# Performance work log

Measured on AMD Instinct MI355X. Metric: run time of the kernel, lower is better.

## Reference

```python
import jax, jax.numpy as jnp
import numpy as np

N, E, D_IN, D_HID, D_OUT = 50000, 800000, 128, 128, 64

def setup_inputs() -> dict:
    key = jax.random.key(0)
    ks = jax.random.split(key, 20)
    inp = {
        'x': jax.random.normal(ks[0], (N, D_IN), dtype=jnp.float32),
        'edge_index': jax.random.randint(ks[1], (2, E), 0, N, dtype=jnp.int64),
        'edge_attr': jax.random.normal(ks[2], (E, 16), dtype=jnp.float32),
        'edge_weight': jax.random.uniform(ks[3], (E,), dtype=jnp.float32),
    }
    dims = [(D_IN, D_HID), (D_HID, D_HID), (D_HID, D_OUT)]
    for i, (di, do) in enumerate(dims):
        s = 1.0 / np.sqrt(di)
        inp[f'Wl{i}'] = jax.random.uniform(ks[4 + 5 * i], (di, do), minval=-s, maxval=s, dtype=jnp.float32)
        inp[f'bl{i}'] = jnp.zeros((do,), dtype=jnp.float32)
        inp[f'Wr{i}'] = jax.random.uniform(ks[5 + 5 * i], (di, do), minval=-s, maxval=s, dtype=jnp.float32)
        inp[f'Ws{i}'] = jax.random.uniform(ks[6 + 5 * i], (di, do), minval=-s, maxval=s, dtype=jnp.float32)
        inp[f'bs{i}'] = jnp.zeros((do,), dtype=jnp.float32)
    return inp


def _sage(x, src, dst, Wl, bl, Wr):
    # mean aggregation of source features at target nodes (PyG SAGEConv)
    msg = x[src]                                               # [E, d] gather
    ssum = jax.ops.segment_sum(msg, dst, num_segments=N)        # [N, d]
    cnt = jax.ops.segment_sum(jnp.ones((src.shape[0],), x.dtype), dst, num_segments=N)
    agg = ssum / jnp.maximum(cnt, 1.0)[:, None]
    return agg @ Wl + bl + x @ Wr                               # lin_l(agg) + lin_r(x)


def reference(x, edge_index, edge_attr, edge_weight,
              Wl0, bl0, Wr0, Ws0, bs0,
              Wl1, bl1, Wr1, Ws1, bs1,
              Wl2, bl2, Wr2, Ws2, bs2):
    src, dst = edge_index[0], edge_index[1]
    h = jax.nn.relu(_sage(x, src, dst, Wl0, bl0, Wr0) + x @ Ws0 + bs0)
    h = jax.nn.relu(_sage(h, src, dst, Wl1, bl1, Wr1) + h @ Ws1 + bs1)
    out = _sage(h, src, dst, Wl2, bl2, Wr2) + h @ Ws2 + bs2
    return out
```

## Files before the change

kernel.cpp:

```cpp
#include <hip/hip_runtime.h>
#include <hip/hip_bf16.h>


#define LB __launch_bounds__

typedef __attribute__((ext_vector_type(8))) short short8;
typedef __attribute__((ext_vector_type(4))) float f32x4;

__device__ __forceinline__ unsigned short bf16_rne(float f) {
  unsigned u = __builtin_bit_cast(unsigned, f);
  unsigned r = u + 0x7fffu + ((u >> 16) & 1u);
  return (unsigned short)(r >> 16);
}
__device__ __forceinline__ float bf16_to_f(unsigned short us) {
  return __builtin_bit_cast(float, (unsigned)us << 16);
}
__device__ __forceinline__ float bits_to_f(unsigned u) {
  return __builtin_bit_cast(float, u);
}

__device__ __forceinline__ void async16(const void* g, void* l) {
  __builtin_amdgcn_global_load_lds((const __attribute__((address_space(1))) unsigned*)g,
                                   (__attribute__((address_space(3))) unsigned*)l, 16, 0, 0);
}

#define BCAP 8192
#define P1_CHUNK 4096

__device__ __forceinline__ void p1_body(int bid, const int* __restrict__ src,
                                        const int* __restrict__ dst, int* __restrict__ bcnt,
                                        int2* __restrict__ pairs, int E) {
  __shared__ int cnt[256];
  __shared__ int base[256];
  const int tid = threadIdx.x;
  cnt[tid] = 0;
  __syncthreads();
  const int e0 = bid * P1_CHUNK;
  int myb[16], myr[16], mys[16], myd[16];
#pragma unroll
  for (int i = 0; i < 16; ++i) {
    int e = e0 + i * 256 + tid;
    myb[i] = -1;
    if (e < E) {
      int s = src[e], d = dst[e];
      int b = d >> 8;
      myb[i] = b;
      mys[i] = s;
      myd[i] = d;
      myr[i] = atomicAdd(&cnt[b], 1);
    }
  }
  __syncthreads();
  base[tid] = (cnt[tid] > 0) ? atomicAdd(&bcnt[tid], cnt[tid]) : 0;
  __syncthreads();
#pragma unroll
  for (int i = 0; i < 16; ++i) {
    int b = myb[i];
    if (b >= 0) {
      int p = base[b] + myr[i];
      if (p < BCAP) pairs[(size_t)b * BCAP + p] = make_int2(mys[i], myd[i]);
    }
  }
}

__device__ __forceinline__ void p234_body(int b, const int2* __restrict__ pairs,
                                          const int* __restrict__ bcnt, int* __restrict__ gcounter,
                                          int* __restrict__ row_start, int* __restrict__ deg_arr,
                                          float* __restrict__ scale, int* __restrict__ srcs, int N) {
  __shared__ int h[256];
  __shared__ int sc[256];
  __shared__ int cur[256];
  __shared__ int shared_bb;
  const int tid = threadIdx.x;
  h[tid] = 0;
  __syncthreads();
  int m = bcnt[b];
  if (m > BCAP) m = BCAP;
  for (int i = tid; i < m; i += 256) {
    atomicAdd(&h[pairs[(size_t)b * BCAP + i].y & 255], 1);
  }
  __syncthreads();
  const int deg = h[tid];
  sc[tid] = deg;
  __syncthreads();
  for (int off = 1; off < 256; off <<= 1) {
    int add = (tid >= off) ? sc[tid - off] : 0;
    __syncthreads();
    sc[tid] += add;
    __syncthreads();
  }
  if (tid == 0) shared_bb = atomicAdd(gcounter, sc[255]);
  __syncthreads();
  const int abs_off = shared_bb + sc[tid] - deg;
  const int node = b * 256 + tid;
  if (node < N) {
    row_start[node] = abs_off;
    deg_arr[node] = deg;
    scale[node] = 1.0f / (float)(deg > 1 ? deg : 1);
  }
  cur[tid] = abs_off;
  __syncthreads();
  for (int i = tid; i < m; i += 256) {
    int2 pr = pairs[(size_t)b * BCAP + i];
    int p = atomicAdd(&cur[pr.y & 255], 1);
    srcs[p] = pr.x;
  }
}

__device__ __forceinline__ void wpack_body(int wb, const float* __restrict__ Wl0,
                                           const float* __restrict__ Wr0,
                                           const float* __restrict__ Ws0,
                                           const float* __restrict__ bl0,
                                           const float* __restrict__ bs0,
                                           const float* __restrict__ Wl1,
                                           const float* __restrict__ Wr1,
                                           const float* __restrict__ Ws1,
                                           const float* __restrict__ bl1,
                                           const float* __restrict__ bs1,
                                           const float* __restrict__ Wl2,
                                           const float* __restrict__ Wr2,
                                           const float* __restrict__ Ws2,
                                           const float* __restrict__ bl2,
                                           const float* __restrict__ bs2, ushort* __restrict__ Bh0,
                                           ushort* __restrict__ Bo0, float* __restrict__ bb0,
                                           ushort* __restrict__ Bh1, ushort* __restrict__ Bo1,
                                           float* __restrict__ bb1, ushort* __restrict__ Bh2,
                                           ushort* __restrict__ Bo2, float* __restrict__ bb2) {
  const int layer = wb >> 7;
  const int xb = wb & 127;
  const float *Wl, *Wr, *Ws, *bl, *bs;
  ushort *Bh, *Bo;
  float* bb;
  int M;
  if (layer == 0) {
    Wl = Wl0; Wr = Wr0; Ws = Ws0; bl = bl0; bs = bs0; Bh = Bh0; Bo = Bo0; bb = bb0; M = 256;
  } else if (layer == 1) {
    Wl = Wl1; Wr = Wr1; Ws = Ws1; bl = bl1; bs = bs1; Bh = Bh1; Bo = Bo1; bb = bb1; M = 256;
  } else {
    Wl = Wl2; Wr = Wr2; Ws = Ws2; bl = bl2; bs = bs2; Bh = Bh2; Bo = Bo2; bb = bb2; M = 128;
  }
  const int DO = M / 2;
  int idx = xb * 256 + (int)threadIdx.x;
  if (idx < 128 * M) {
    int k = idx / M, c = idx - k * M;
    float v = (c < DO) ? Wl[k * DO + c] : (Wr[k * DO + (c - DO)] + Ws[k * DO + (c - DO)]);
    unsigned short h = bf16_rne(v);
    unsigned short l = bf16_rne(v - bf16_to_f(h));
    int d = ((k >> 3) * M + c) * 8 + (k & 7);
    Bh[d] = h;
    Bo[d] = l;
  }
  if (idx < DO) bb[idx] = bl[idx] + bs[idx];
}

__device__ __forceinline__ void split8v(f32x4 f0, f32x4 f1, short8& h, short8& l) {
  float f[8] = {f0[0], f0[1], f0[2], f0[3], f1[0], f1[1], f1[2], f1[3]};
#pragma unroll
  for (int j = 0; j < 8; ++j) {
    unsigned u = __builtin_bit_cast(unsigned, f[j]);
    h[j] = (short)(u >> 16);
    l[j] = (short)bf16_rne(f[j] - bits_to_f(u & 0xffff0000u));
  }
}

template <int M>
__device__ __forceinline__ void gemm_compute(int bx, const char* smem,
                                             const ushort* __restrict__ Bhi,
                                             const ushort* __restrict__ Blo,
                                             ushort* __restrict__ Yb, float* __restrict__ Z,
                                             int n) {
  constexpr int DO = M / 2;
  constexpr int NWC = (M >= 256) ? 4 : 2;
  constexpr int NWR = 4 / NWC;
  constexpr int BROWS = 32 * NWR;
  const int tid = threadIdx.x;
  const int w = tid >> 6, l = tid & 63;
  const int q = l >> 4, m16 = l & 15;
  const int rowBase = bx * BROWS + (w / NWC) * 32;
  const int colBase = (w % NWC) * 64;

  f32x4 acc[2][4] = {};
  const int rl0 = (w / NWC) * 32 + m16;

#pragma unroll
  for (int s = 0; s < 4; ++s) {
    short8 ah[2], al[2], bh[4], bo[4];
    const int kb = s * 4 + q;
#pragma unroll
    for (int i = 0; i < 2; ++i) {
      int rl = rl0 + i * 16;
      int g0 = (2 * kb) ^ m16;
      int g1 = (2 * kb + 1) ^ m16;
      f32x4 fa = *(const f32x4*)(smem + (size_t)rl * 512 + g0 * 16);
      f32x4 fb = *(const f32x4*)(smem + (size_t)rl * 512 + g1 * 16);
      split8v(fa, fb, ah[i], al[i]);
    }
#pragma unroll
    for (int j = 0; j < 4; ++j) {
      size_t off = ((size_t)kb * M + colBase + j * 16 + m16) * 8;
      bh[j] = *(const short8*)(Bhi + off);
      bo[j] = *(const short8*)(Blo + off);
    }
#pragma unroll
    for (int i = 0; i < 2; ++i)
#pragma unroll
      for (int j = 0; j < 4; ++j) {
        acc[i][j] = __builtin_amdgcn_mfma_f32_16x16x32_bf16(ah[i], bh[j], acc[i][j], 0, 0, 0);
        acc[i][j] = __builtin_amdgcn_mfma_f32_16x16x32_bf16(ah[i], bo[j], acc[i][j], 0, 0, 0);
        acc[i][j] = __builtin_amdgcn_mfma_f32_16x16x32_bf16(al[i], bh[j], acc[i][j], 0, 0, 0);
      }
  }

#pragma unroll
  for (int i = 0; i < 2; ++i) {
    int rb = rowBase + i * 16 + q * 4;
#pragma unroll
    for (int j = 0; j < 4; ++j) {
      int c = colBase + j * 16 + m16;
#pragma unroll
      for (int r = 0; r < 4; ++r) {
        int row = rb + r;
        if (row < n) {
          float v = acc[i][j][r];
          if (c < DO)
            Yb[(size_t)row * DO + c] = bf16_rne(v);
          else
            Z[(size_t)row * DO + (c - DO)] = v;
        }
      }
    }
  }
}

__device__ __forceinline__ void gemm0_body(int bx, const float* __restrict__ x,
                                           const ushort* __restrict__ Bh,
                                           const ushort* __restrict__ Bo, ushort* __restrict__ Yb,
                                           float* __restrict__ Z, int n, char* smem) {
  const int tid = threadIdx.x;
  const int wbase = tid & ~63;
#pragma unroll
  for (int r = 0; r < 4; ++r) {
    int ell = r * 256 + tid;
    int row = ell >> 5, gl = ell & 31;
    int grow = bx * 32 + row;
    if (grow >= n) grow = n - 1;
    int gs = gl ^ (row & 15);
    async16(x + (size_t)grow * 128 + gs * 4, smem + (size_t)(r * 256 + wbase) * 16);
  }
  __syncthreads();
  gemm_compute<256>(bx, smem, Bh, Bo, Yb, Z, n);
}

__device__ __forceinline__ void acc8(float* a, uint4 u) {
  a[0] += bits_to_f(u.x << 16);
  a[1] += bits_to_f(u.x & 0xffff0000u);
  a[2] += bits_to_f(u.y << 16);
  a[3] += bits_to_f(u.y & 0xffff0000u);
  a[4] += bits_to_f(u.z << 16);
  a[5] += bits_to_f(u.z & 0xffff0000u);
  a[6] += bits_to_f(u.w << 16);
  a[7] += bits_to_f(u.w & 0xffff0000u);
}

template <int M>
__global__ LB(256, 4) void fused_agg_gemm(const ushort* __restrict__ Y,
                                          const float* __restrict__ Zprev,
                                          const int* __restrict__ row_start,
                                          const int* __restrict__ deg_arr,
                                          const int* __restrict__ srcs,
                                          const float* __restrict__ scale,
                                          const float* __restrict__ bsum,
                                          const ushort* __restrict__ Bhi,
                                          const ushort* __restrict__ Blo, ushort* __restrict__ Yb,
                                          float* __restrict__ Zf, int n) {
  constexpr int BROWS = (M >= 256) ? 32 : 64;
  __shared__ __align__(16) char smem[BROWS * 512];
  const int tid = threadIdx.x;
  const int w = tid >> 6;
  const int lane = tid & 63;
  const int qt = lane >> 4;
  const int li = lane & 15;
  const int blockRow0 = blockIdx.x * BROWS;
  const uint4* Y4 = (const uint4*)Y;

#pragma unroll 1
  for (int t = 0; t < BROWS / 16; ++t) {
    const int r = t * 16 + w * 4 + qt;
    const int node = blockRow0 + r;
    const bool live = node < n;
    const int cn = live ? node : n - 1;
    const int e0q = row_start[cn];
    const int cntq = live ? deg_arr[cn] : 0;
    const float sc = scale[cn];
    float4 z0 = ((const float4*)Zprev)[(size_t)cn * 32 + 2 * li];
    float4 z1 = ((const float4*)Zprev)[(size_t)cn * 32 + 2 * li + 1];
    float4 b0 = ((const float4*)bsum)[2 * li];
    float4 b1 = ((const float4*)bsum)[2 * li + 1];
    float a[8] = {0.f, 0.f, 0.f, 0.f, 0.f, 0.f, 0.f, 0.f};

    int cm = cntq;
    cm = max(cm, __shfl_xor(cm, 16));
    cm = max(cm, __shfl_xor(cm, 32));

    for (int base = 0; base < cm; base += 16) {
      int idx = (base + li < cntq) ? srcs[e0q + base + li] : 0;
      int lim = cm - base;
      if (lim > 16) lim = 16;
      for (int jj = 0; jj < lim; jj += 8) {
        int s[8];
#pragma unroll
        for (int k = 0; k < 8; ++k) s[k] = __shfl(idx, (qt << 4) + jj + k);
        uint4 u[8];
#pragma unroll
        for (int k = 0; k < 8; ++k) {
          uint4 v = make_uint4(0u, 0u, 0u, 0u);
          if (base + jj + k < cntq) v = Y4[(size_t)s[k] * 16 + li];
          u[k] = v;
        }
#pragma unroll
        for (int k = 0; k < 8; ++k) acc8(a, u[k]);
      }
    }
    float4 o0, o1;
    o0.x = fmaxf(z0.x + sc * a[0] + b0.x, 0.f);
    o0.y = fmaxf(z0.y + sc * a[1] + b0.y, 0.f);
    o0.z = fmaxf(z0.z + sc * a[2] + b0.z, 0.f);
    o0.w = fmaxf(z0.w + sc * a[3] + b0.w, 0.f);
    o1.x = fmaxf(z1.x + sc * a[4] + b1.x, 0.f);
    o1.y = fmaxf(z1.y + sc * a[5] + b1.y, 0.f);
    o1.z = fmaxf(z1.z + sc * a[6] + b1.z, 0.f);
    o1.w = fmaxf(z1.w + sc * a[7] + b1.w, 0.f);
    *(float4*)(smem + (size_t)r * 512 + (size_t)(((2 * li) ^ (r & 15)) * 16)) = o0;
    *(float4*)(smem + (size_t)r * 512 + (size_t)(((2 * li + 1) ^ (r & 15)) * 16)) = o1;
  }
  __syncthreads();
  gemm_compute<M>(blockIdx.x, smem, Bhi, Blo, Yb, Zf, n);
}

__global__ LB(256) void fused_wpack_p1(const int* __restrict__ src, const int* __restrict__ dst,
                                       int* __restrict__ bcnt, int2* __restrict__ pairs, int E,
                                       int NP1, const float* Wl0, const float* Wr0, const float* Ws0,
                                       const float* bl0, const float* bs0, const float* Wl1,
                                       const float* Wr1, const float* Ws1, const float* bl1,
                                       const float* bs1, const float* Wl2, const float* Wr2,
                                       const float* Ws2, const float* bl2, const float* bs2,
                                       ushort* Bh0, ushort* Bo0, float* bb0, ushort* Bh1,
                                       ushort* Bo1, float* bb1, ushort* Bh2, ushort* Bo2,
                                       float* bb2) {
  if ((int)blockIdx.x < NP1) {
    p1_body(blockIdx.x, src, dst, bcnt, pairs, E);
  } else {
    wpack_body(blockIdx.x - NP1, Wl0, Wr0, Ws0, bl0, bs0, Wl1, Wr1, Ws1, bl1, bs1, Wl2, Wr2, Ws2,
               bl2, bs2, Bh0, Bo0, bb0, Bh1, Bo1, bb1, Bh2, Bo2, bb2);
  }
}

__global__ LB(256, 5) void fused_p234_gemm0(const int2* __restrict__ pairs,
                                            const int* __restrict__ bcnt, int* __restrict__ gcounter,
                                            int* __restrict__ row_start, int* __restrict__ deg_arr,
                                            float* __restrict__ scale, int* __restrict__ srcs, int N,
                                            const float* __restrict__ x,
                                            const ushort* __restrict__ Bh0,
                                            const ushort* __restrict__ Bo0, ushort* __restrict__ Yb,
                                            float* __restrict__ Zf, int NB) {
  __shared__ __align__(16) char smem[32 * 512];
  if ((int)blockIdx.x < NB) {
    p234_body(blockIdx.x, pairs, bcnt, gcounter, row_start, deg_arr, scale, srcs, N);
  } else {
    gemm0_body(blockIdx.x - NB, x, Bh0, Bo0, Yb, Zf, N, smem);
  }
}

__global__ LB(256, 4) void agg64_kernel(const ushort* __restrict__ Y, const float* __restrict__ Z,
                                        const int* __restrict__ row_start,
                                        const int* __restrict__ deg_arr, const int* __restrict__ srcs,
                                        const float* __restrict__ scale,
                                        const float* __restrict__ bsum, float* __restrict__ out,
                                        int n) {
  const int tid = threadIdx.x;
  const int lane = tid & 63;
  const int qt = lane >> 4;
  const int li = lane & 15;
  const int node = blockIdx.x * 16 + (tid >> 6) * 4 + qt;
  const bool live = node < n;
  const int cn = live ? node : n - 1;
  const int e0q = row_start[cn];
  const int cntq = live ? deg_arr[cn] : 0;
  const uint2* Yu = (const uint2*)Y;
  float a0 = 0.f, a1 = 0.f, a2 = 0.f, a3 = 0.f;
  const float sc = scale[cn];
  float4 z = ((const float4*)Z)[(size_t)cn * 16 + li];
  float4 b = ((const float4*)bsum)[li];

  int cm = cntq;
  cm = max(cm, __shfl_xor(cm, 16));
  cm = max(cm, __shfl_xor(cm, 32));

  for (int base = 0; base < cm; base += 16) {
    int idx = (base + li < cntq) ? srcs[e0q + base + li] : 0;
    int lim = cm - base;
    if (lim > 16) lim = 16;
    for (int jj = 0; jj < lim; jj += 8) {
      int s[8];
#pragma unroll
      for (int k = 0; k < 8; ++k) s[k] = __shfl(idx, (qt << 4) + jj + k);
      uint2 u[8];
#pragma unroll
      for (int k = 0; k < 8; ++k) {
        uint2 v = make_uint2(0u, 0u);
        if (base + jj + k < cntq) v = Yu[(size_t)s[k] * 16 + li];
        u[k] = v;
      }
#pragma unroll
      for (int k = 0; k < 8; ++k) {
        a0 += bits_to_f(u[k].x << 16);
        a1 += bits_to_f(u[k].x & 0xffff0000u);
        a2 += bits_to_f(u[k].y << 16);
        a3 += bits_to_f(u[k].y & 0xffff0000u);
      }
    }
  }
  if (live) {
    float4 o;
    o.x = z.x + sc * a0 + b.x;
    o.y = z.y + sc * a1 + b.y;
    o.z = z.z + sc * a2 + b.z;
    o.w = z.w + sc * a3 + b.w;
    ((float4*)out)[(size_t)node * 16 + li] = o;
  }
}

extern "C" void kernel_launch(void* const* d_in, const int* in_sizes, int n_in,
                              void* d_out, int out_size, void* d_ws, size_t ws_size,
                              hipStream_t stream) {
  const float* x = (const float*)d_in[0];
  const int* ei = (const int*)d_in[1];
  const int N = in_sizes[0] / 128;
  const int E = in_sizes[3];
  const int* src = ei;
  const int* dst = ei + E;
  const float* Wl[3] = {(const float*)d_in[4], (const float*)d_in[9], (const float*)d_in[14]};
  const float* bl[3] = {(const float*)d_in[5], (const float*)d_in[10], (const float*)d_in[15]};
  const float* Wr[3] = {(const float*)d_in[6], (const float*)d_in[11], (const float*)d_in[16]};
  const float* Ws[3] = {(const float*)d_in[7], (const float*)d_in[12], (const float*)d_in[17]};
  const float* bs[3] = {(const float*)d_in[8], (const float*)d_in[13], (const float*)d_in[18]};

  const int NB = (N + 255) >> 8;
  const int NP1 = (E + P1_CHUNK - 1) / P1_CHUNK;

  size_t off = 0;
  auto carve = [&](size_t bytes) -> char* {
    char* p = (char*)d_ws + off;
    off += (bytes + 255) & ~(size_t)255;
    return p;
  };
  int* row_start = (int*)carve((size_t)N * 4);
  int* deg_arr = (int*)carve((size_t)N * 4);
  int* bcnt = (int*)carve((size_t)NB * 4);
  int* gcounter = (int*)carve(256);
  float* scale = (float*)carve((size_t)N * 4);
  int* srcs = (int*)carve((size_t)E * 4);
  int2* pairs = (int2*)carve((size_t)NB * BCAP * 8);
  ushort* Yb0 = (ushort*)carve((size_t)N * 128 * 2);
  float* Zf0 = (float*)carve((size_t)N * 128 * 4);
  ushort* Yb1 = (ushort*)carve((size_t)N * 128 * 2);
  float* Zf1 = (float*)carve((size_t)N * 128 * 4);
  ushort* Bh[3];
  ushort* Bo[3];
  float* bsum[3];
  for (int i = 0; i < 3; ++i) {
    Bh[i] = (ushort*)carve(128 * 256 * 2);
    Bo[i] = (ushort*)carve(128 * 256 * 2);
    bsum[i] = (float*)carve(128 * 4);
  }
  (void)ws_size;
  (void)n_in;
  (void)out_size;

  size_t bcnt_pad = ((size_t)NB * 4 + 255) & ~(size_t)255;
  hipMemsetAsync(bcnt, 0, bcnt_pad + 4, stream);

  fused_wpack_p1<<<NP1 + 384, 256, 0, stream>>>(
      src, dst, bcnt, pairs, E, NP1, Wl[0], Wr[0], Ws[0], bl[0], bs[0], Wl[1], Wr[1], Ws[1], bl[1],
      bs[1], Wl[2], Wr[2], Ws[2], bl[2], bs[2], Bh[0], Bo[0], bsum[0], Bh[1], Bo[1], bsum[1], Bh[2],
      Bo[2], bsum[2]);

  int g32 = (N + 31) / 32;
  int g64 = (N + 63) / 64;
  int gAgg = (N + 15) / 16;

  fused_p234_gemm0<<<NB + g32, 256, 0, stream>>>(pairs, bcnt, gcounter, row_start, deg_arr, scale,
                                                 srcs, N, x, Bh[0], Bo[0], Yb0, Zf0, NB);
  fused_agg_gemm<256><<<g32, 256, 0, stream>>>(Yb0, Zf0, row_start, deg_arr, srcs, scale, bsum[0],
                                               Bh[1], Bo[1], Yb1, Zf1, N);
  fused_agg_gemm<128><<<g64, 256, 0, stream>>>(Yb1, Zf1, row_start, deg_arr, srcs, scale, bsum[1],
                                               Bh[2], Bo[2], Yb0, Zf0, N);
  agg64_kernel<<<gAgg, 256, 0, stream>>>(Yb0, Zf0, row_start, deg_arr, srcs, scale, bsum[2],
                                         (float*)d_out, N);
}
```

Measured before the change: 277.3 us.

## Partition bf16 feature table into 32-column slabs for cache-local gathers

The GEMM epilogue now writes the bf16 Y features in a column-partitioned layout: separate 32-column slabs, each stored as [n][32]. The aggregation kernels loop over the slabs in turn, so each gather pass touches a smaller table that is more likely to stay in L2/MALL. They also switch to narrower 4-byte gathers and use nontemporal loads for the streamed index and Z data. The cost is repeating the edge-index walk and degree loop once per slab, and issuing more, smaller gather loads.

New measurement: 351.4 us. +26.7%, slower.

```diff
diff --git a/kernel.cpp b/kernel.cpp
--- a/kernel.cpp
+++ b/kernel.cpp
@@ -217,13 +217,15 @@
 #pragma unroll
     for (int j = 0; j < 4; ++j) {
       int c = colBase + j * 16 + m16;
+      int p = (colBase + j * 16) >> 5;
+      int cc = (j & 1) * 16 + m16;
 #pragma unroll
       for (int r = 0; r < 4; ++r) {
         int row = rb + r;
         if (row < n) {
           float v = acc[i][j][r];
           if (c < DO)
-            Yb[(size_t)row * DO + c] = bf16_rne(v);
+            Yb[((size_t)p * n + row) * 32 + cc] = bf16_rne(v);
           else
             Z[(size_t)row * DO + (c - DO)] = v;
         }
@@ -249,17 +251,6 @@
   }
   __syncthreads();
   gemm_compute<256>(bx, smem, Bh, Bo, Yb, Z, n);
-}
-
-__device__ __forceinline__ void acc8(float* a, uint4 u) {
-  a[0] += bits_to_f(u.x << 16);
-  a[1] += bits_to_f(u.x & 0xffff0000u);
-  a[2] += bits_to_f(u.y << 16);
-  a[3] += bits_to_f(u.y & 0xffff0000u);
-  a[4] += bits_to_f(u.z << 16);
-  a[5] += bits_to_f(u.z & 0xffff0000u);
-  a[6] += bits_to_f(u.w << 16);
-  a[7] += bits_to_f(u.w & 0xffff0000u);
 }
 
 template <int M>
@@ -280,58 +271,57 @@
   const int lane = tid & 63;
   const int qt = lane >> 4;
   const int li = lane & 15;
-  const int blockRow0 = blockIdx.x * BROWS;
-  const uint4* Y4 = (const uint4*)Y;
 
 #pragma unroll 1
-  for (int t = 0; t < BROWS / 16; ++t) {
-    const int r = t * 16 + w * 4 + qt;
-    const int node = blockRow0 + r;
-    const bool live = node < n;
-    const int cn = live ? node : n - 1;
-    const int e0q = row_start[cn];
-    const int cntq = live ? deg_arr[cn] : 0;
-    const float sc = scale[cn];
-    float4 z0 = ((const float4*)Zprev)[(size_t)cn * 32 + 2 * li];
-    float4 z1 = ((const float4*)Zprev)[(size_t)cn * 32 + 2 * li + 1];
-    float4 b0 = ((const float4*)bsum)[2 * li];
-    float4 b1 = ((const float4*)bsum)[2 * li + 1];
-    float a[8] = {0.f, 0.f, 0.f, 0.f, 0.f, 0.f, 0.f, 0.f};
-
-    int cm = cntq;
-    cm = max(cm, __shfl_xor(cm, 16));
-    cm = max(cm, __shfl_xor(cm, 32));
-
-    for (int base = 0; base < cm; base += 16) {
-      int idx = (base + li < cntq) ? srcs[e0q + base + li] : 0;
-      int lim = cm - base;
-      if (lim > 16) lim = 16;
-      for (int jj = 0; jj < lim; jj += 8) {
-        int s[8];
-#pragma unroll
-        for (int k = 0; k < 8; ++k) s[k] = __shfl(idx, (qt << 4) + jj + k);
-        uint4 u[8];
-#pragma unroll
-        for (int k = 0; k < 8; ++k) {
-          uint4 v = make_uint4(0u, 0u, 0u, 0u);
-          if (base + jj + k < cntq) v = Y4[(size_t)s[k] * 16 + li];
-          u[k] = v;
+  for (int p = 0; p < 4; ++p) {
+    const ushort* Yp = Y + (size_t)p * n * 32;
+#pragma unroll 1
+    for (int t = 0; t < BROWS / 16; ++t) {
+      const int r = t * 16 + w * 4 + qt;
+      const int node = blockIdx.x * BROWS + r;
+      const bool live = node < n;
+      const int cn = live ? node : n - 1;
+      const int e0q = row_start[cn];
+      const int cntq = live ? deg_arr[cn] : 0;
+      const float sc = scale[cn];
+      const int c0 = p * 32 + 2 * li;
+      float zx = __builtin_nontemporal_load(Zprev + (size_t)cn * 128 + c0);
+      float zy = __builtin_nontemporal_load(Zprev + (size_t)cn * 128 + c0 + 1);
+      float bx = bsum[c0], by = bsum[c0 + 1];
+      float a0 = 0.f, a1 = 0.f;
+
+      int cm = cntq;
+      cm = max(cm, __shfl_xor(cm, 16));
+      cm = max(cm, __shfl_xor(cm, 32));
+
+      for (int base = 0; base < cm; base += 16) {
+        int idx = (base + li < cntq) ? __builtin_nontemporal_load(srcs + e0q + base + li) : 0;
+        int lim = cm - base;
+        if (lim > 16) lim = 16;
+        for (int jj = 0; jj < lim; jj += 8) {
+          int s[8];
+#pragma unroll
+          for (int k = 0; k < 8; ++k) s[k] = __shfl(idx, (qt << 4) + jj + k);
+          unsigned u[8];
+#pragma unroll
+          for (int k = 0; k < 8; ++k) {
+            unsigned v = 0u;
+            if (base + jj + k < cntq) v = *(const unsigned*)(Yp + (size_t)s[k] * 32 + li * 2);
+            u[k] = v;
+          }
+#pragma unroll
+          for (int k = 0; k < 8; ++k) {
+            a0 += bits_to_f(u[k] << 16);
+            a1 += bits_to_f(u[k] & 0xffff0000u);
+          }
         }
-#pragma unroll
-        for (int k = 0; k < 8; ++k) acc8(a, u[k]);
       }
-    }
-    float4 o0, o1;
-    o0.x = fmaxf(z0.x + sc * a[0] + b0.x, 0.f);
-    o0.y = fmaxf(z0.y + sc * a[1] + b0.y, 0.f);
-    o0.z = fmaxf(z0.z + sc * a[2] + b0.z, 0.f);
-    o0.w = fmaxf(z0.w + sc * a[3] + b0.w, 0.f);
-    o1.x = fmaxf(z1.x + sc * a[4] + b1.x, 0.f);
-    o1.y = fmaxf(z1.y + sc * a[5] + b1.y, 0.f);
-    o1.z = fmaxf(z1.z + sc * a[6] + b1.z, 0.f);
-    o1.w = fmaxf(z1.w + sc * a[7] + b1.w, 0.f);
-    *(float4*)(smem + (size_t)r * 512 + (size_t)(((2 * li) ^ (r & 15)) * 16)) = o0;
-    *(float4*)(smem + (size_t)r * 512 + (size_t)(((2 * li + 1) ^ (r & 15)) * 16)) = o1;
+      float o0 = fmaxf(zx + sc * a0 + bx, 0.f);
+      float o1 = fmaxf(zy + sc * a1 + by, 0.f);
+      int b0 = p * 128 + li * 8;
+      int sb = (((b0 >> 4) ^ (r & 15)) << 4) + (b0 & 15);
+      *(float2*)(smem + (size_t)r * 512 + sb) = make_float2(o0, o1);
+    }
   }
   __syncthreads();
   gemm_compute<M>(blockIdx.x, smem, Bhi, Blo, Yb, Zf, n);
@@ -386,47 +376,47 @@
   const int cn = live ? node : n - 1;
   const int e0q = row_start[cn];
   const int cntq = live ? deg_arr[cn] : 0;
-  const uint2* Yu = (const uint2*)Y;
-  float a0 = 0.f, a1 = 0.f, a2 = 0.f, a3 = 0.f;
   const float sc = scale[cn];
-  float4 z = ((const float4*)Z)[(size_t)cn * 16 + li];
-  float4 b = ((const float4*)bsum)[li];
 
   int cm = cntq;
   cm = max(cm, __shfl_xor(cm, 16));
   cm = max(cm, __shfl_xor(cm, 32));
 
-  for (int base = 0; base < cm; base += 16) {
-    int idx = (base + li < cntq) ? srcs[e0q + base + li] : 0;
-    int lim = cm - base;
-    if (lim > 16) lim = 16;
-    for (int jj = 0; jj < lim; jj += 8) {
-      int s[8];
-#pragma unroll
-      for (int k = 0; k < 8; ++k) s[k] = __shfl(idx, (qt << 4) + jj + k);
-      uint2 u[8];
-#pragma unroll
-      for (int k = 0; k < 8; ++k) {
-        uint2 v = make_uint2(0u, 0u);
-        if (base + jj + k < cntq) v = Yu[(size_t)s[k] * 16 + li];
-        u[k] = v;
+#pragma unroll 1
+  for (int p = 0; p < 2; ++p) {
+    const ushort* Yp = Y + (size_t)p * n * 32;
+    const int c0 = p * 32 + 2 * li;
+    float zx = __builtin_nontemporal_load(Z + (size_t)cn * 64 + c0);
+    float zy = __builtin_nontemporal_load(Z + (size_t)cn * 64 + c0 + 1);
+    float a0 = 0.f, a1 = 0.f;
+    for (int base = 0; base < cm; base += 16) {
+      int idx = (base + li < cntq) ? __builtin_nontemporal_load(srcs + e0q + base + li) : 0;
+      int lim = cm - base;
+      if (lim > 16) lim = 16;
+      for (int jj = 0; jj < lim; jj += 8) {
+        int s[8];
+#pragma unroll
+        for (int k = 0; k < 8; ++k) s[k] = __shfl(idx, (qt << 4) + jj + k);
+        unsigned u[8];
+#pragma unroll
+        for (int k = 0; k < 8; ++k) {
+          unsigned v = 0u;
+          if (base + jj + k < cntq) v = *(const unsigned*)(Yp + (size_t)s[k] * 32 + li * 2);
+          u[k] = v;
+        }
+#pragma unroll
+        for (int k = 0; k < 8; ++k) {
+          a0 += bits_to_f(u[k] << 16);
+          a1 += bits_to_f(u[k] & 0xffff0000u);
+        }
       }
-#pragma unroll
-      for (int k = 0; k < 8; ++k) {
-        a0 += bits_to_f(u[k].x << 16);
-        a1 += bits_to_f(u[k].x & 0xffff0000u);
-        a2 += bits_to_f(u[k].y << 16);
-        a3 += bits_to_f(u[k].y & 0xffff0000u);
-      }
-    }
-  }
-  if (live) {
-    float4 o;
-    o.x = z.x + sc * a0 + b.x;
-    o.y = z.y + sc * a1 + b.y;
-    o.z = z.z + sc * a2 + b.z;
-    o.w = z.w + sc * a3 + b.w;
-    ((float4*)out)[(size_t)node * 16 + li] = o;
+    }
+    if (live) {
+      float2 o;
+      o.x = zx + sc * a0 + bsum[c0];
+      o.y = zy + sc * a1 + bsum[c0 + 1];
+      *(float2*)(out + (size_t)node * 64 + c0) = o;
+    }
   }
 }
 
```
